# Optimization experiments

Hardware: AMD Instinct MI355X
Metric: run time of the kernel (lower is better)

## Reference

```python
import jax, jax.numpy as jnp
import numpy as np
import math

EMBED = 512
HEADS = 8
HEAD_DIM = EMBED // HEADS
PATCH = 4
IMG = 32
NP_SIDE = IMG // PATCH          # 8
NUM_PATCHES = NP_SIDE * NP_SIDE  # 64
SEQ = NUM_PATCHES + 1            # 65
PATCH_FEAT = PATCH * PATCH * 3   # 48
HID = 1024
NCLS = 10
B = 2048


def setup_inputs() -> dict:
    key = jax.random.key(0)
    ks = jax.random.split(key, 14)
    s = lambda fan_in: 1.0 / math.sqrt(fan_in)
    return {
        "x": jax.random.normal(ks[0], (B, 3, IMG, IMG), dtype=jnp.float32),
        "proj_w": jax.random.uniform(ks[1], (EMBED, PATCH_FEAT), minval=-s(PATCH_FEAT), maxval=s(PATCH_FEAT)),
        "proj_b": jax.random.uniform(ks[2], (EMBED,), minval=-s(PATCH_FEAT), maxval=s(PATCH_FEAT)),
        "cls": jax.random.normal(ks[3], (1, 1, EMBED), dtype=jnp.float32),
        "pos": jax.random.normal(ks[4], (SEQ, EMBED), dtype=jnp.float32),
        "wq": jax.random.uniform(ks[5], (HEADS, HEAD_DIM, EMBED), minval=-s(EMBED), maxval=s(EMBED)),
        "bq": jax.random.uniform(ks[6], (HEADS, HEAD_DIM), minval=-s(EMBED), maxval=s(EMBED)),
        "wo": jax.random.uniform(ks[7], (EMBED, EMBED), minval=-s(EMBED), maxval=s(EMBED)),
        "bo": jax.random.uniform(ks[8], (EMBED,), minval=-s(EMBED), maxval=s(EMBED)),
        "w1": jax.random.uniform(ks[9], (HID, EMBED), minval=-s(EMBED), maxval=s(EMBED)),
        "b1": jax.random.uniform(ks[10], (HID,), minval=-s(EMBED), maxval=s(EMBED)),
        "w2": jax.random.uniform(ks[11], (NCLS, HID), minval=-s(HID), maxval=s(HID)),
        "b2": jax.random.uniform(ks[12], (NCLS,), minval=-s(HID), maxval=s(HID)),
    }


def reference(x, proj_w, proj_b, cls, pos, wq, bq, wo, bo, w1, b1, w2, b2):
    b = x.shape[0]
    # nn.Unfold(kernel=4, stride=4): per-patch vector ordered (C, kh, kw)
    p = x.reshape(b, 3, NP_SIDE, PATCH, NP_SIDE, PATCH)
    p = p.transpose(0, 2, 4, 1, 3, 5).reshape(b, NUM_PATCHES, PATCH_FEAT)
    emb = p @ proj_w.T + proj_b                                   # [B, 64, 512]
    seq = jnp.concatenate([jnp.broadcast_to(cls, (b, 1, EMBED)), emb], axis=1)
    seq = seq + pos                                               # [B, 65, 512]

    # Faithful bug: q, k, v all come from the query projection
    q = jnp.einsum('bsd,hkd->bhsk', seq, wq) + bq[None, :, None, :]  # [B,H,S,Dh]
    w = jnp.einsum('bhsk,bhtk->bhst', q, q) / math.sqrt(HEAD_DIM)
    # Faithful bug: softmax over dim=1 of [B,S,S] per head -> query axis (axis=2 here)
    w = jax.nn.softmax(w, axis=2)
    att = jnp.einsum('bhst,bhtk->bhsk', w, q)                     # [B,H,S,Dh]
    mh = att.transpose(0, 2, 1, 3).reshape(b, SEQ, EMBED)
    out = mh @ wo.T + bo                                          # [B, 65, 512]

    ct = out[:, 0, :]
    h = jax.nn.gelu(ct @ w1.T + b1, approximate=False)
    logits = h @ w2.T + b2                                        # [B, 10]
    return logits
```

## Files before the change

### kernel.cpp

```cpp
#include <hip/hip_runtime.h>
#include <hip/hip_bf16.h>
#include <math.h>

#define BATCH 2048
#define SEQL 65
#define EMB 512
#define NHEADS 8
#define HD 64
#define NPATCH 64
#define PFEAT 48
#define HIDDIM 1024
#define NCLS 10

typedef short bfrag __attribute__((ext_vector_type(8)));
typedef float facc  __attribute__((ext_vector_type(16)));

union B8 { unsigned int u[4]; unsigned long long ull[2]; bfrag f; };

__device__ inline unsigned int cvt2(float a, float b) {
  __hip_bfloat162 t = __float22bfloat162_rn(float2{a, b});
  return *(unsigned int*)&t;
}
__device__ inline unsigned short f2bf(float f) {
  __hip_bfloat16 h = __float2bfloat16(f);
  return *(unsigned short*)&h;
}
__device__ inline float bf2f(unsigned short h) {
  return __uint_as_float(((unsigned int)h) << 16);
}
__device__ inline float lo16f(unsigned int u) { return __uint_as_float(u << 16); }
__device__ inline float hi16f(unsigned int u) { return __uint_as_float(u & 0xffff0000u); }
__device__ inline bfrag ldf(const unsigned short* p) {
  union { unsigned long long u[2]; bfrag s; } c;
  c.u[0] = *(const unsigned long long*)(p);
  c.u[1] = *(const unsigned long long*)(p + 4);
  return c.s;
}

__global__ __launch_bounds__(256) void k_prep(
    const float* __restrict__ wq, const float* __restrict__ proj_w,
    unsigned short* __restrict__ WcH, unsigned short* __restrict__ WcL,
    const float* __restrict__ wo, unsigned short* __restrict__ WoH,
    unsigned short* __restrict__ WoL,
    const float* __restrict__ w1, unsigned short* __restrict__ W1H,
    unsigned short* __restrict__ W1L,
    float* __restrict__ wqT)
{
  __shared__ float sm[1088];
  const int bid = blockIdx.x, tid = threadIdx.x;
  if (bid < 512) {
    float* wr = sm;
    float* part = sm + 512;
    const int hk = bid;
    wr[tid]     = wq[(size_t)hk*EMB + tid];
    wr[256+tid] = wq[(size_t)hk*EMB + 256 + tid];
    __syncthreads();
    if (tid < PFEAT*4) {
      int f = tid % PFEAT, p = tid / PFEAT;
      float a = 0.f;
      for (int d = p*128; d < (p+1)*128; ++d) a += wr[d]*proj_w[d*PFEAT + f];
      part[p*PFEAT + f] = a;
    }
    __syncthreads();
    if (tid < PFEAT) {
      float v = part[tid] + part[PFEAT+tid] + part[2*PFEAT+tid] + part[3*PFEAT+tid];
      unsigned short hi = f2bf(v);
      WcH[hk*PFEAT + tid] = hi;
      WcL[hk*PFEAT + tid] = f2bf(v - bf2f(hi));
    }
  } else if (bid < 1536) {
    int i = (bid - 512)*256 + tid;
    float v = wo[i];
    unsigned short hi = f2bf(v);
    WoH[i] = hi; WoL[i] = f2bf(v - bf2f(hi));
  } else if (bid < 3584) {
    int i = (bid - 1536)*256 + tid;
    float v = w1[i];
    unsigned short hi = f2bf(v);
    W1H[i] = hi; W1L[i] = f2bf(v - bf2f(hi));
  } else {
    float (*t)[33] = (float(*)[33])sm;
    const int r = bid - 3584, bx = (r & 15)*32, by = (r >> 4)*32;
    const int c = tid & 31, r0 = tid >> 5;
    #pragma unroll
    for (int i = 0; i < 4; ++i) {
      int rr = r0 + 8*i;
      t[rr][c] = wq[(size_t)(by + rr)*512 + bx + c];
    }
    __syncthreads();
    #pragma unroll
    for (int i = 0; i < 4; ++i) {
      int rr = r0 + 8*i;
      wqT[(size_t)(bx + rr)*512 + by + c] = t[c][rr];
    }
  }
}

__global__ __launch_bounds__(256) void k_qbias(
    const float* __restrict__ wqT, const float* __restrict__ bq,
    const float* __restrict__ cls, const float* __restrict__ pos,
    const float* __restrict__ proj_b, float* __restrict__ qbias)
{
  __shared__ float v[EMB];
  __shared__ float part[256];
  const int h = blockIdx.x / SEQL, s = blockIdx.x - h*SEQL;
  const int tid = threadIdx.x;
  const float* po = pos + (size_t)s*EMB;
  v[tid]     = po[tid]     + (s == 0 ? cls[tid]     : proj_b[tid]);
  v[256+tid] = po[256+tid] + (s == 0 ? cls[256+tid] : proj_b[256+tid]);
  __syncthreads();
  const int p = tid >> 6, k = tid & 63;
  const float* wp = wqT + h*HD + k;
  float a = 0.f;
  for (int d = p*128; d < p*128 + 128; ++d)
    a = fmaf(v[d], wp[(size_t)d*512], a);
  part[p*64 + k] = a;
  __syncthreads();
  if (tid < HD)
    qbias[((size_t)h*SEQL + s)*HD + tid] =
        part[tid] + part[64+tid] + part[128+tid] + part[192+tid] + bq[h*HD + tid];
}

__global__ __launch_bounds__(256) void k_attn(
    const float* __restrict__ x, const unsigned short* __restrict__ WcH,
    const unsigned short* __restrict__ WcL, const float* __restrict__ qbias,
    unsigned short* __restrict__ mh0H, unsigned short* __restrict__ mh0L)
{
  __shared__ __align__(16) char smem[19456];
  unsigned short* Qh = (unsigned short*)smem;
  float* mpart = (float*)(smem + 13056);
  float* spart = (float*)(smem + 15360);
  float* S0    = (float*)(smem + 17664);
  float* p0v   = (float*)(smem + 18048);
  float* attp  = (float*)(smem + 18432);

  const int b = blockIdx.x & 2047, h = blockIdx.x >> 11;
  const int tid = threadIdx.x, w = tid >> 6, lane = tid & 63;
  const int u2 = lane >> 5;
  const float* xb = x + (size_t)b*3072;
  const float* qb = qbias + (size_t)h*SEQL*HD;
  const float C = 0.18033688011112042f;

  {
    const int ti = w >> 1, tj = w & 1;
    const int ar = 32*ti + (lane & 31);
    const int ni = ar >> 3, nj = ar & 7;
    const float* pbase = xb + (ni*4 + 2*u2)*32 + nj*4;
    const int br = 32*tj + (lane & 31);
    const unsigned short* whp = WcH + ((size_t)(h*HD + br))*PFEAT;
    const unsigned short* wlp = WcL + ((size_t)(h*HD + br))*PFEAT;
    facc acc = {0,0,0,0,0,0,0,0,0,0,0,0,0,0,0,0};
    #pragma unroll
    for (int ks = 0; ks < 3; ++ks) {
      float4 va = *(const float4*)(pbase + ks*1024);
      float4 vb = *(const float4*)(pbase + ks*1024 + 32);
      B8 ah, al;
      ah.u[0] = cvt2(va.x, va.y); ah.u[1] = cvt2(va.z, va.w);
      ah.u[2] = cvt2(vb.x, vb.y); ah.u[3] = cvt2(vb.z, vb.w);
      al.u[0] = cvt2(va.x - lo16f(ah.u[0]), va.y - hi16f(ah.u[0]));
      al.u[1] = cvt2(va.z - lo16f(ah.u[1]), va.w - hi16f(ah.u[1]));
      al.u[2] = cvt2(vb.x - lo16f(ah.u[2]), vb.y - hi16f(ah.u[2]));
      al.u[3] = cvt2(vb.z - lo16f(ah.u[3]), vb.w - hi16f(ah.u[3]));
      const int f0 = ks*16 + u2*8;
      B8 bh, bl;
      bh.f = *(const bfrag*)(whp + f0);
      bl.f = *(const bfrag*)(wlp + f0);
      acc = __builtin_amdgcn_mfma_f32_32x32x16_bf16(ah.f, bh.f, acc, 0, 0, 0);
      acc = __builtin_amdgcn_mfma_f32_32x32x16_bf16(ah.f, bl.f, acc, 0, 0, 0);
      acc = __builtin_amdgcn_mfma_f32_32x32x16_bf16(al.f, bh.f, acc, 0, 0, 0);
    }
    #pragma unroll
    for (int r = 0; r < 16; ++r) {
      int row = (r & 3) + 8*(r >> 2) + 4*u2 + 32*ti;
      int s = 1 + row;
      Qh[s*68 + br] = f2bf(acc[r] + qb[s*HD + br]);
    }
    if (tid < HD) Qh[tid] = f2bf(qb[tid]);
    for (int i = tid; i < 31*17; i += 256) {
      int row = 65 + i/17, o = (i - (i/17)*17)*4;
      *(unsigned long long*)(Qh + row*68 + o) = 0ull;
    }
  }
  __syncthreads();

  for (int t = w; t < 9; t += 4) {
    const int ri = t/3, ci = t - ri*3;
    const int ar2 = 32*ri + (lane & 31);
    const int br2 = 32*ci + (lane & 31);
    facc a2 = {0,0,0,0,0,0,0,0,0,0,0,0,0,0,0,0};
    #pragma unroll
    for (int ks = 0; ks < 4; ++ks) {
      int k0 = ks*16 + u2*8;
      bfrag qa = ldf(Qh + ar2*68 + k0);
      bfrag qc = ldf(Qh + br2*68 + k0);
      a2 = __builtin_amdgcn_mfma_f32_32x32x16_bf16(qa, qc, a2, 0, 0, 0);
    }
    float m, s;
    if (ri == 2) {
      m = (u2 == 0) ? a2[0] : -3.0e38f;
      s = (u2 == 0) ? 1.0f : 0.0f;
    } else {
      m = a2[0];
      #pragma unroll
      for (int r = 1; r < 16; ++r) m = fmaxf(m, a2[r]);
      float mm = m * C;
      s = 0.f;
      #pragma unroll
      for (int r = 0; r < 16; ++r)
        s += __builtin_amdgcn_exp2f(fmaf(a2[r], C, -mm));
    }
    const int pi = ri*2 + u2;
    mpart[pi*96 + br2] = m;
    spart[pi*96 + br2] = s;
    if (ri == 0 && u2 == 0) S0[br2] = a2[0];
  }
  __syncthreads();

  if (tid < SEQL) {
    float m = mpart[tid];
    #pragma unroll
    for (int i = 1; i < 6; ++i) m = fmaxf(m, mpart[i*96 + tid]);
    float mm = m * C;
    float s = 0.f;
    #pragma unroll
    for (int i = 0; i < 6; ++i)
      s += spart[i*96 + tid] * __builtin_amdgcn_exp2f(fmaf(mpart[i*96 + tid], C, -mm));
    p0v[tid] = __builtin_amdgcn_exp2f(fmaf(S0[tid], C, -mm)) / s;
  }
  __syncthreads();

  {
    int k = tid & 63, p = tid >> 6;
    int t0 = p*17, t1 = (t0 + 17 < SEQL) ? t0 + 17 : SEQL;
    float a = 0.f;
    for (int t = t0; t < t1; ++t)
      a += p0v[t] * bf2f(Qh[t*68 + k]);
    attp[p*64 + k] = a;
  }
  __syncthreads();
  if (tid < HD) {
    float a = attp[tid] + attp[64+tid] + attp[128+tid] + attp[192+tid];
    unsigned short hi = f2bf(a);
    mh0H[(size_t)b*EMB + h*HD + tid] = hi;
    mh0L[(size_t)b*EMB + h*HD + tid] = f2bf(a - bf2f(hi));
  }
}

template<bool GELU>
__global__ __launch_bounds__(256) void k_gemm(
    const unsigned short* __restrict__ AH, const unsigned short* __restrict__ AL,
    const unsigned short* __restrict__ WH, const unsigned short* __restrict__ WL,
    const float* __restrict__ bias, float* __restrict__ Cf,
    unsigned short* __restrict__ CH, unsigned short* __restrict__ CL,
    int N, int K)
{
  __shared__ float red[4096];
  const int tid = threadIdx.x, w = tid >> 6, lane = tid & 63;
  const int u2 = lane >> 5;
  const int m0 = blockIdx.x*32, n0 = blockIdx.y*32;
  const int kb = w*(K >> 2);
  const unsigned short* ahp = AH + (size_t)(m0 + (lane & 31))*K + kb + u2*8;
  const unsigned short* alp = AL + (size_t)(m0 + (lane & 31))*K + kb + u2*8;
  const unsigned short* bhp = WH + (size_t)(n0 + (lane & 31))*K + kb + u2*8;
  const unsigned short* blp = WL + (size_t)(n0 + (lane & 31))*K + kb + u2*8;
  facc acc = {0,0,0,0,0,0,0,0,0,0,0,0,0,0,0,0};
  const int kc = K >> 2;
  for (int k = 0; k < kc; k += 16) {
    bfrag ah = *(const bfrag*)(ahp + k);
    bfrag al = *(const bfrag*)(alp + k);
    bfrag bh = *(const bfrag*)(bhp + k);
    bfrag bl = *(const bfrag*)(blp + k);
    acc = __builtin_amdgcn_mfma_f32_32x32x16_bf16(ah, bh, acc, 0, 0, 0);
    acc = __builtin_amdgcn_mfma_f32_32x32x16_bf16(ah, bl, acc, 0, 0, 0);
    acc = __builtin_amdgcn_mfma_f32_32x32x16_bf16(al, bh, acc, 0, 0, 0);
  }
  #pragma unroll
  for (int r = 0; r < 16; ++r) red[(w*16 + r)*64 + lane] = acc[r];
  __syncthreads();
  #pragma unroll
  for (int e0 = 0; e0 < 4; ++e0) {
    int e = e0*256 + tid;
    int r = e >> 6, l = e & 63;
    float c = red[e] + red[1024+e] + red[2048+e] + red[3072+e];
    int row = m0 + (r & 3) + 8*(r >> 2) + 4*(l >> 5);
    int col = n0 + (l & 31);
    c += bias[col];
    if (GELU) {
      c = 0.5f*c*(1.f + erff(c*0.70710678118654752f));
      Cf[(size_t)row*N + col] = c;
    } else {
      unsigned short hi = f2bf(c);
      CH[(size_t)row*N + col] = hi;
      CL[(size_t)row*N + col] = f2bf(c - bf2f(hi));
    }
  }
}

__global__ __launch_bounds__(256) void k_logits(
    const float* __restrict__ hh, const float* __restrict__ w2,
    const float* __restrict__ b2, float* __restrict__ out)
{
  const int w = threadIdx.x >> 6, lane = threadIdx.x & 63;
  const int r = blockIdx.x*4 + w;
  const float* hr = hh + (size_t)r*HIDDIM + lane*16;
  float hv[16];
  #pragma unroll
  for (int i4 = 0; i4 < 4; ++i4) {
    float4 v = *(const float4*)(hr + i4*4);
    hv[i4*4+0] = v.x; hv[i4*4+1] = v.y; hv[i4*4+2] = v.z; hv[i4*4+3] = v.w;
  }
  float acc[NCLS];
  #pragma unroll
  for (int c = 0; c < NCLS; ++c) {
    const float* wr = w2 + (size_t)c*HIDDIM + lane*16;
    float a = 0.f;
    #pragma unroll
    for (int i4 = 0; i4 < 4; ++i4) {
      float4 wv = *(const float4*)(wr + i4*4);
      a += hv[i4*4]*wv.x + hv[i4*4+1]*wv.y + hv[i4*4+2]*wv.z + hv[i4*4+3]*wv.w;
    }
    acc[c] = a;
  }
  #pragma unroll
  for (int c = 0; c < NCLS; ++c)
    #pragma unroll
    for (int m = 1; m < 64; m <<= 1) acc[c] += __shfl_xor(acc[c], m, 64);
  if (lane == 0) {
    #pragma unroll
    for (int c = 0; c < NCLS; ++c) out[(size_t)r*NCLS + c] = acc[c] + b2[c];
  }
}

extern "C" void kernel_launch(void* const* d_in, const int* in_sizes, int n_in,
                              void* d_out, int out_size, void* d_ws, size_t ws_size,
                              hipStream_t stream)
{
  const float* x      = (const float*)d_in[0];
  const float* proj_w = (const float*)d_in[1];
  const float* proj_b = (const float*)d_in[2];
  const float* cls    = (const float*)d_in[3];
  const float* pos    = (const float*)d_in[4];
  const float* wq     = (const float*)d_in[5];
  const float* bq     = (const float*)d_in[6];
  const float* wo     = (const float*)d_in[7];
  const float* bo     = (const float*)d_in[8];
  const float* w1     = (const float*)d_in[9];
  const float* b1     = (const float*)d_in[10];
  const float* w2     = (const float*)d_in[11];
  const float* b2     = (const float*)d_in[12];
  float* out = (float*)d_out;

  unsigned short* WcH = (unsigned short*)d_ws;
  unsigned short* WcL = (unsigned short*)((char*)d_ws + 49152);
  float* qbias        = (float*)((char*)d_ws + 98304);
  unsigned short* WoH = (unsigned short*)((char*)d_ws + 231424);
  unsigned short* WoL = (unsigned short*)((char*)d_ws + 755712);
  unsigned short* W1H = (unsigned short*)((char*)d_ws + 1280000);
  unsigned short* W1L = (unsigned short*)((char*)d_ws + 2328576);
  unsigned short* mh0H = (unsigned short*)((char*)d_ws + 3377152);
  unsigned short* mh0L = (unsigned short*)((char*)d_ws + 5474304);
  unsigned short* ctH  = (unsigned short*)((char*)d_ws + 7571456);
  unsigned short* ctL  = (unsigned short*)((char*)d_ws + 9668608);
  float* hh           = (float*)((char*)d_ws + 11765760);
  float* wqT          = hh;

  hipLaunchKernelGGL(k_prep, dim3(3840), dim3(256), 0, stream,
                     wq, proj_w, WcH, WcL, wo, WoH, WoL, w1, W1H, W1L, wqT);
  hipLaunchKernelGGL(k_qbias, dim3(NHEADS*SEQL), dim3(256), 0, stream,
                     wqT, bq, cls, pos, proj_b, qbias);
  hipLaunchKernelGGL(k_attn, dim3(BATCH*NHEADS), dim3(256), 0, stream,
                     x, WcH, WcL, qbias, mh0H, mh0L);
  hipLaunchKernelGGL((k_gemm<false>), dim3(BATCH/32, EMB/32), dim3(256), 0, stream,
                     mh0H, mh0L, WoH, WoL, bo, (float*)nullptr, ctH, ctL, EMB, EMB);
  hipLaunchKernelGGL((k_gemm<true>),  dim3(BATCH/32, HIDDIM/32), dim3(256), 0, stream,
                     ctH, ctL, W1H, W1L, b1, hh, (unsigned short*)nullptr,
                     (unsigned short*)nullptr, HIDDIM, EMB);
  hipLaunchKernelGGL(k_logits, dim3(BATCH/4), dim3(256), 0, stream,
                     hh, w2, b2, out);
}
```

Before: 275.4 us.

## Fold output projection into first MLP weight and retile the MLP GEMM

Precomputes W1·Wo and the combined bias W1·bo + b1 once per call, so the batch-sized Wo GEMM and its bf16 hi/lo intermediate disappear. The remaining MLP GEMM now uses 64x64 tiles staged through shared memory instead of per-wave K-splitting with a reduction step. This adds a 1024x512x512 weight-product kernel and changes the rounding order, since the split-bf16 precision is applied to the fused weight rather than to each factor separately.

```diff
diff --git a/kernel.cpp b/kernel.cpp
--- a/kernel.cpp
+++ b/kernel.cpp
@@ -36,14 +36,18 @@
   c.u[1] = *(const unsigned long long*)(p + 4);
   return c.s;
 }
+__device__ inline void split8(const float* v, B8& h, B8& l) {
+  h.u[0] = cvt2(v[0], v[1]); h.u[1] = cvt2(v[2], v[3]);
+  h.u[2] = cvt2(v[4], v[5]); h.u[3] = cvt2(v[6], v[7]);
+  l.u[0] = cvt2(v[0]-lo16f(h.u[0]), v[1]-hi16f(h.u[0]));
+  l.u[1] = cvt2(v[2]-lo16f(h.u[1]), v[3]-hi16f(h.u[1]));
+  l.u[2] = cvt2(v[4]-lo16f(h.u[2]), v[5]-hi16f(h.u[2]));
+  l.u[3] = cvt2(v[6]-lo16f(h.u[3]), v[7]-hi16f(h.u[3]));
+}
 
 __global__ __launch_bounds__(256) void k_prep(
     const float* __restrict__ wq, const float* __restrict__ proj_w,
     unsigned short* __restrict__ WcH, unsigned short* __restrict__ WcL,
-    const float* __restrict__ wo, unsigned short* __restrict__ WoH,
-    unsigned short* __restrict__ WoL,
-    const float* __restrict__ w1, unsigned short* __restrict__ W1H,
-    unsigned short* __restrict__ W1L,
     float* __restrict__ wqT)
 {
   __shared__ float sm[1088];
@@ -68,19 +72,9 @@
       WcH[hk*PFEAT + tid] = hi;
       WcL[hk*PFEAT + tid] = f2bf(v - bf2f(hi));
     }
-  } else if (bid < 1536) {
-    int i = (bid - 512)*256 + tid;
-    float v = wo[i];
-    unsigned short hi = f2bf(v);
-    WoH[i] = hi; WoL[i] = f2bf(v - bf2f(hi));
-  } else if (bid < 3584) {
-    int i = (bid - 1536)*256 + tid;
-    float v = w1[i];
-    unsigned short hi = f2bf(v);
-    W1H[i] = hi; W1L[i] = f2bf(v - bf2f(hi));
   } else {
     float (*t)[33] = (float(*)[33])sm;
-    const int r = bid - 3584, bx = (r & 15)*32, by = (r >> 4)*32;
+    const int r = bid - 512, bx = (r & 15)*32, by = (r >> 4)*32;
     const int c = tid & 31, r0 = tid >> 5;
     #pragma unroll
     for (int i = 0; i < 4; ++i) {
@@ -119,6 +113,77 @@
   if (tid < HD)
     qbias[((size_t)h*SEQL + s)*HD + tid] =
         part[tid] + part[64+tid] + part[128+tid] + part[192+tid] + bq[h*HD + tid];
+}
+
+__global__ __launch_bounds__(256) void k_fuse(
+    const float* __restrict__ w1, const float* __restrict__ wo,
+    unsigned short* __restrict__ W1cH, unsigned short* __restrict__ W1cL)
+{
+  __shared__ float woT[64*65];
+  const int tid = threadIdx.x, w = tid >> 6, lane = tid & 63;
+  const int u2 = lane >> 5;
+  const int i0 = blockIdx.x*64, d0 = blockIdx.y*64;
+  const int ti = w >> 1, tj = w & 1;
+  const int ar = i0 + 32*ti + (lane & 31);
+  const int brl = 32*tj + (lane & 31);
+  const int jr = tid >> 3, d4 = (tid & 7)*8;
+  facc acc = {0,0,0,0,0,0,0,0,0,0,0,0,0,0,0,0};
+  for (int j0 = 0; j0 < EMB; j0 += 64) {
+    __syncthreads();
+    #pragma unroll
+    for (int p = 0; p < 2; ++p) {
+      int j = j0 + p*32 + jr;
+      const float* wp = wo + (size_t)j*EMB + d0 + d4;
+      float4 v0 = *(const float4*)(wp);
+      float4 v1 = *(const float4*)(wp + 4);
+      int jc = p*32 + jr;
+      woT[(d4+0)*65 + jc] = v0.x; woT[(d4+1)*65 + jc] = v0.y;
+      woT[(d4+2)*65 + jc] = v0.z; woT[(d4+3)*65 + jc] = v0.w;
+      woT[(d4+4)*65 + jc] = v1.x; woT[(d4+5)*65 + jc] = v1.y;
+      woT[(d4+6)*65 + jc] = v1.z; woT[(d4+7)*65 + jc] = v1.w;
+    }
+    __syncthreads();
+    #pragma unroll
+    for (int ks = 0; ks < 4; ++ks) {
+      const int jf = ks*16 + u2*8;
+      const float* ap = w1 + (size_t)ar*EMB + j0 + jf;
+      float4 a0 = *(const float4*)(ap);
+      float4 a1 = *(const float4*)(ap + 4);
+      float av[8] = {a0.x,a0.y,a0.z,a0.w,a1.x,a1.y,a1.z,a1.w};
+      float bv[8];
+      #pragma unroll
+      for (int e = 0; e < 8; ++e) bv[e] = woT[brl*65 + jf + e];
+      B8 ah, al, bh, bl;
+      split8(av, ah, al); split8(bv, bh, bl);
+      acc = __builtin_amdgcn_mfma_f32_32x32x16_bf16(ah.f, bh.f, acc, 0, 0, 0);
+      acc = __builtin_amdgcn_mfma_f32_32x32x16_bf16(ah.f, bl.f, acc, 0, 0, 0);
+      acc = __builtin_amdgcn_mfma_f32_32x32x16_bf16(al.f, bh.f, acc, 0, 0, 0);
+    }
+  }
+  #pragma unroll
+  for (int r = 0; r < 16; ++r) {
+    int row = i0 + 32*ti + (r & 3) + 8*(r >> 2) + 4*u2;
+    int col = d0 + brl;
+    float v = acc[r];
+    unsigned short hi = f2bf(v);
+    W1cH[(size_t)row*EMB + col] = hi;
+    W1cL[(size_t)row*EMB + col] = f2bf(v - bf2f(hi));
+  }
+}
+
+__global__ __launch_bounds__(256) void k_b1c(
+    const float* __restrict__ w1, const float* __restrict__ bo,
+    const float* __restrict__ b1, float* __restrict__ b1c)
+{
+  int i = blockIdx.x*256 + threadIdx.x;
+  const float* wr = w1 + (size_t)i*EMB;
+  float a = b1[i];
+  for (int j = 0; j < EMB; j += 4) {
+    float4 wv = *(const float4*)(wr + j);
+    float4 bv = *(const float4*)(bo + j);
+    a += wv.x*bv.x + wv.y*bv.y + wv.z*bv.z + wv.w*bv.w;
+  }
+  b1c[i] = a;
 }
 
 __global__ __launch_bounds__(256) void k_attn(
@@ -246,53 +311,62 @@
   }
 }
 
-template<bool GELU>
-__global__ __launch_bounds__(256) void k_gemm(
+__global__ __launch_bounds__(256) void k_gemm2(
     const unsigned short* __restrict__ AH, const unsigned short* __restrict__ AL,
-    const unsigned short* __restrict__ WH, const unsigned short* __restrict__ WL,
-    const float* __restrict__ bias, float* __restrict__ Cf,
-    unsigned short* __restrict__ CH, unsigned short* __restrict__ CL,
-    int N, int K)
-{
-  __shared__ float red[4096];
+    const unsigned short* __restrict__ BH, const unsigned short* __restrict__ BL,
+    const float* __restrict__ bias, float* __restrict__ C, int N, int K)
+{
+  __shared__ __align__(16) unsigned short sAh[64*68];
+  __shared__ __align__(16) unsigned short sAl[64*68];
+  __shared__ __align__(16) unsigned short sBh[64*68];
+  __shared__ __align__(16) unsigned short sBl[64*68];
   const int tid = threadIdx.x, w = tid >> 6, lane = tid & 63;
   const int u2 = lane >> 5;
-  const int m0 = blockIdx.x*32, n0 = blockIdx.y*32;
-  const int kb = w*(K >> 2);
-  const unsigned short* ahp = AH + (size_t)(m0 + (lane & 31))*K + kb + u2*8;
-  const unsigned short* alp = AL + (size_t)(m0 + (lane & 31))*K + kb + u2*8;
-  const unsigned short* bhp = WH + (size_t)(n0 + (lane & 31))*K + kb + u2*8;
-  const unsigned short* blp = WL + (size_t)(n0 + (lane & 31))*K + kb + u2*8;
+  const int m0 = blockIdx.x*64, n0 = blockIdx.y*64;
+  const int ti = w >> 1, tj = w & 1;
+  const int arl = 32*ti + (lane & 31);
+  const int brl = 32*tj + (lane & 31);
+  const int srow = tid >> 3, scol = (tid & 7)*8;
   facc acc = {0,0,0,0,0,0,0,0,0,0,0,0,0,0,0,0};
-  const int kc = K >> 2;
-  for (int k = 0; k < kc; k += 16) {
-    bfrag ah = *(const bfrag*)(ahp + k);
-    bfrag al = *(const bfrag*)(alp + k);
-    bfrag bh = *(const bfrag*)(bhp + k);
-    bfrag bl = *(const bfrag*)(blp + k);
-    acc = __builtin_amdgcn_mfma_f32_32x32x16_bf16(ah, bh, acc, 0, 0, 0);
-    acc = __builtin_amdgcn_mfma_f32_32x32x16_bf16(ah, bl, acc, 0, 0, 0);
-    acc = __builtin_amdgcn_mfma_f32_32x32x16_bf16(al, bh, acc, 0, 0, 0);
+  for (int k0 = 0; k0 < K; k0 += 64) {
+    __syncthreads();
+    #pragma unroll
+    for (int p = 0; p < 2; ++p) {
+      int row = p*32 + srow;
+      B8 va, vb, vc, vd;
+      va.f = *(const bfrag*)(AH + (size_t)(m0+row)*K + k0 + scol);
+      vb.f = *(const bfrag*)(AL + (size_t)(m0+row)*K + k0 + scol);
+      vc.f = *(const bfrag*)(BH + (size_t)(n0+row)*K + k0 + scol);
+      vd.f = *(const bfrag*)(BL + (size_t)(n0+row)*K + k0 + scol);
+      *(unsigned long long*)(sAh + row*68 + scol)     = va.ull[0];
+      *(unsigned long long*)(sAh + row*68 + scol + 4) = va.ull[1];
+      *(unsigned long long*)(sAl + row*68 + scol)     = vb.ull[0];
+      *(unsigned long long*)(sAl + row*68 + scol + 4) = vb.ull[1];
+      *(unsigned long long*)(sBh + row*68 + scol)     = vc.ull[0];
+      *(unsigned long long*)(sBh + row*68 + scol + 4) = vc.ull[1];
+      *(unsigned long long*)(sBl + row*68 + scol)     = vd.ull[0];
+      *(unsigned long long*)(sBl + row*68 + scol + 4) = vd.ull[1];
+    }
+    __syncthreads();
+    #pragma unroll
+    for (int ks = 0; ks < 4; ++ks) {
+      int jf = ks*16 + u2*8;
+      bfrag ah = ldf(sAh + arl*68 + jf);
+      bfrag al = ldf(sAl + arl*68 + jf);
+      bfrag bh = ldf(sBh + brl*68 + jf);
+      bfrag bl = ldf(sBl + brl*68 + jf);
+      acc = __builtin_amdgcn_mfma_f32_32x32x16_bf16(ah, bh, acc, 0, 0, 0);
+      acc = __builtin_amdgcn_mfma_f32_32x32x16_bf16(ah, bl, acc, 0, 0, 0);
+      acc = __builtin_amdgcn_mfma_f32_32x32x16_bf16(al, bh, acc, 0, 0, 0);
+    }
   }
   #pragma unroll
-  for (int r = 0; r < 16; ++r) red[(w*16 + r)*64 + lane] = acc[r];
-  __syncthreads();
-  #pragma unroll
-  for (int e0 = 0; e0 < 4; ++e0) {
-    int e = e0*256 + tid;
-    int r = e >> 6, l = e & 63;
-    float c = red[e] + red[1024+e] + red[2048+e] + red[3072+e];
-    int row = m0 + (r & 3) + 8*(r >> 2) + 4*(l >> 5);
-    int col = n0 + (l & 31);
-    c += bias[col];
-    if (GELU) {
-      c = 0.5f*c*(1.f + erff(c*0.70710678118654752f));
-      Cf[(size_t)row*N + col] = c;
-    } else {
-      unsigned short hi = f2bf(c);
-      CH[(size_t)row*N + col] = hi;
-      CL[(size_t)row*N + col] = f2bf(c - bf2f(hi));
-    }
+  for (int r = 0; r < 16; ++r) {
+    int row = m0 + 32*ti + (r & 3) + 8*(r >> 2) + 4*u2;
+    int col = n0 + brl;
+    float c = acc[r] + bias[col];
+    c = 0.5f*c*(1.f + erff(c*0.70710678118654752f));
+    C[(size_t)row*N + col] = c;
   }
 }
 
@@ -350,31 +424,29 @@
   const float* b2     = (const float*)d_in[12];
   float* out = (float*)d_out;
 
-  unsigned short* WcH = (unsigned short*)d_ws;
-  unsigned short* WcL = (unsigned short*)((char*)d_ws + 49152);
-  float* qbias        = (float*)((char*)d_ws + 98304);
-  unsigned short* WoH = (unsigned short*)((char*)d_ws + 231424);
-  unsigned short* WoL = (unsigned short*)((char*)d_ws + 755712);
-  unsigned short* W1H = (unsigned short*)((char*)d_ws + 1280000);
-  unsigned short* W1L = (unsigned short*)((char*)d_ws + 2328576);
-  unsigned short* mh0H = (unsigned short*)((char*)d_ws + 3377152);
-  unsigned short* mh0L = (unsigned short*)((char*)d_ws + 5474304);
-  unsigned short* ctH  = (unsigned short*)((char*)d_ws + 7571456);
-  unsigned short* ctL  = (unsigned short*)((char*)d_ws + 9668608);
-  float* hh           = (float*)((char*)d_ws + 11765760);
-  float* wqT          = hh;
-
-  hipLaunchKernelGGL(k_prep, dim3(3840), dim3(256), 0, stream,
-                     wq, proj_w, WcH, WcL, wo, WoH, WoL, w1, W1H, W1L, wqT);
+  unsigned short* WcH  = (unsigned short*)d_ws;
+  unsigned short* WcL  = (unsigned short*)((char*)d_ws + 49152);
+  float* qbias         = (float*)((char*)d_ws + 98304);
+  unsigned short* W1cH = (unsigned short*)((char*)d_ws + 231424);
+  unsigned short* W1cL = (unsigned short*)((char*)d_ws + 1280000);
+  float* b1c           = (float*)((char*)d_ws + 2328576);
+  unsigned short* mh0H = (unsigned short*)((char*)d_ws + 2332672);
+  unsigned short* mh0L = (unsigned short*)((char*)d_ws + 4429824);
+  float* hh            = (float*)((char*)d_ws + 6526976);
+  float* wqT           = hh;
+
+  hipLaunchKernelGGL(k_prep, dim3(768), dim3(256), 0, stream,
+                     wq, proj_w, WcH, WcL, wqT);
   hipLaunchKernelGGL(k_qbias, dim3(NHEADS*SEQL), dim3(256), 0, stream,
                      wqT, bq, cls, pos, proj_b, qbias);
+  hipLaunchKernelGGL(k_fuse, dim3(HIDDIM/64, EMB/64), dim3(256), 0, stream,
+                     w1, wo, W1cH, W1cL);
+  hipLaunchKernelGGL(k_b1c, dim3(HIDDIM/256), dim3(256), 0, stream,
+                     w1, bo, b1, b1c);
   hipLaunchKernelGGL(k_attn, dim3(BATCH*NHEADS), dim3(256), 0, stream,
                      x, WcH, WcL, qbias, mh0H, mh0L);
-  hipLaunchKernelGGL((k_gemm<false>), dim3(BATCH/32, EMB/32), dim3(256), 0, stream,
-                     mh0H, mh0L, WoH, WoL, bo, (float*)nullptr, ctH, ctL, EMB, EMB);
-  hipLaunchKernelGGL((k_gemm<true>),  dim3(BATCH/32, HIDDIM/32), dim3(256), 0, stream,
-                     ctH, ctL, W1H, W1L, b1, hh, (unsigned short*)nullptr,
-                     (unsigned short*)nullptr, HIDDIM, EMB);
+  hipLaunchKernelGGL(k_gemm2, dim3(BATCH/64, HIDDIM/64), dim3(256), 0, stream,
+                     mh0H, mh0L, W1cH, W1cL, b1c, hh, HIDDIM, EMB);
   hipLaunchKernelGGL(k_logits, dim3(BATCH/4), dim3(256), 0, stream,
                      hh, w2, b2, out);
 }
```

Result: faster. 252.6 us (-8.3%).
